# Kernel tuning notes

Measured on AMD Instinct MI355X. Metric: run time of the kernel, lower is better.

The kernel has to match this reference:

```python
import jax, jax.numpy as jnp
import numpy as np

N_NODES = 50000


def _gcn_layer(x, src, dst, norm_src, norm_dst, W, b, act):
    # DGL GraphConv with norm='both': D_out^{-1/2} A D_in^{-1/2} X W + b
    h = x * norm_src[:, None]                      # scale by src out-degree
    m = h[src]                                     # gather messages [E, d]
    agg = jax.ops.segment_sum(m, dst, num_segments=N_NODES)  # scatter-add
    agg = agg * norm_dst[:, None]
    out = agg @ W + b
    if act:
        out = jax.nn.relu(out)
    return out


def setup_inputs() -> dict:
    key = jax.random.key(0)
    ks = jax.random.split(key, 10)
    E = 800000
    in_size, hid, out_size = 128, 128, 64
    features = jax.random.normal(ks[0], (N_NODES, in_size), dtype=jnp.float32)
    src = jax.random.randint(ks[1], (E,), 0, N_NODES, dtype=jnp.int32)
    dst = jax.random.randint(ks[2], (E,), 0, N_NODES, dtype=jnp.int32)
    s = 0.05
    W1 = jax.random.normal(ks[3], (in_size, hid), dtype=jnp.float32) * s
    b1 = jnp.zeros((hid,), dtype=jnp.float32)
    W2 = jax.random.normal(ks[4], (hid, hid), dtype=jnp.float32) * s
    b2 = jnp.zeros((hid,), dtype=jnp.float32)
    W3 = jax.random.normal(ks[5], (hid, out_size), dtype=jnp.float32) * s
    b3 = jnp.zeros((out_size,), dtype=jnp.float32)
    return {"features": features, "W1": W1, "b1": b1, "W2": W2, "b2": b2,
            "W3": W3, "b3": b3, "src": src, "dst": dst}


def reference(features, W1, b1, W2, b2, W3, b3, src, dst):
    ones = jnp.ones(src.shape, dtype=features.dtype)
    out_deg = jax.ops.segment_sum(ones, src, num_segments=N_NODES)
    in_deg = jax.ops.segment_sum(ones, dst, num_segments=N_NODES)
    norm_src = jnp.maximum(out_deg, 1.0) ** -0.5   # clamp(min=1) as in DGL
    norm_dst = jnp.maximum(in_deg, 1.0) ** -0.5
    h = _gcn_layer(features, src, dst, norm_src, norm_dst, W1, b1, act=True)
    # dropout is identity in eval mode
    h = _gcn_layer(h, src, dst, norm_src, norm_dst, W2, b2, act=True)
    h = _gcn_layer(h, src, dst, norm_src, norm_dst, W3, b3, act=False)
    return h
```

## Files before the change

### kernel.cpp

```cpp
#include <hip/hip_runtime.h>
#include <math.h>

#define N_NODES 50000
#define K_DIM 128
#define CAP 64
#define CHUNK 25000
#define RH 25000
#define HWORDS 12500

typedef __attribute__((ext_vector_type(8))) short short8_t;
typedef __attribute__((ext_vector_type(4))) float f32x4_t;
typedef __attribute__((ext_vector_type(8))) _Float16 half8_t;

__device__ inline unsigned short f2bf(float x) {
    unsigned u = __float_as_uint(x);
    unsigned r = u + 0x7fffu + ((u >> 16) & 1u);
    return (unsigned short)(r >> 16);
}
__device__ inline float bf2f(unsigned short h) {
    return __uint_as_float(((unsigned)h) << 16);
}

__global__ void init_zero_kernel(_Float16* Yx, _Float16* Yy, _Float16* Yz) {
    int t = threadIdx.x;
    if (t < 128) {
        Yx[(size_t)N_NODES * 128 + t] = (_Float16)0.f;
        Yy[(size_t)N_NODES * 128 + t] = (_Float16)0.f;
    }
    if (t < 64) Yz[(size_t)N_NODES * 64 + t] = (_Float16)0.f;
}


__global__ __launch_bounds__(1024) void hist_kernel(const int* __restrict__ src,
                                                    const int* __restrict__ dst, int E,
                                                    unsigned* __restrict__ pin,
                                                    unsigned* __restrict__ pout) {
    __shared__ unsigned h[HWORDS];
    int b  = blockIdx.x >> 2;
    int io = (blockIdx.x >> 1) & 1;
    int r  = blockIdx.x & 1;
    int tid = threadIdx.x;
    for (int t = tid; t < HWORDS; t += 1024) h[t] = 0;
    __syncthreads();
    const int* keys = io ? src : dst;
    int start = b * CHUNK;
    int end = start + CHUNK; if (end > E) end = E;
    int vlo = r * RH;
    for (int i = start + tid; i < end; i += 1024) {
        int v = keys[i] - vlo;
        if ((unsigned)v < (unsigned)RH)
            atomicAdd(&h[v >> 1], 1u << ((v & 1) * 16));
    }
    __syncthreads();
    unsigned* out = io ? pout : pin;
    for (int t = tid; t < HWORDS; t += 1024)
        out[(size_t)b * (2 * HWORDS) + r * HWORDS + t] = h[t];
}

__global__ void offsets_norm_kernel(const unsigned* __restrict__ pin,
                                    const unsigned* __restrict__ pout,
                                    unsigned short* __restrict__ off16,
                                    int* __restrict__ indeg,
                                    float* __restrict__ nsrc, float* __restrict__ ndst,
                                    int n, int NB) {
    int v = blockIdx.x * blockDim.x + threadIdx.x;
    if (v >= n) return;
    int wi = v >> 1, sh = (v & 1) * 16;
    int od = 0;
    for (int b = 0; b < NB; ++b)
        od += (pout[(size_t)b * (2 * HWORDS) + wi] >> sh) & 0xffff;
    int run = 0;
    for (int b = 0; b < NB; ++b) {
        int c = (pin[(size_t)b * (2 * HWORDS) + wi] >> sh) & 0xffff;
        off16[(size_t)b * n + v] = (unsigned short)(run < CAP ? run : CAP);
        run += c;
    }
    indeg[v] = run < CAP ? run : CAP;
    int odc = od < 1 ? 1 : od;
    int idc = run < 1 ? 1 : run;
    nsrc[v] = 1.0f / sqrtf((float)odc);
    ndst[v] = 1.0f / sqrtf((float)idc);
}

__global__ __launch_bounds__(1024) void scatter_kernel(const int* __restrict__ src,
                                                       const int* __restrict__ dst, int E,
                                                       const unsigned short* __restrict__ off16,
                                                       int* __restrict__ csr, int n) {
    __shared__ unsigned cur[HWORDS];
    int b = blockIdx.x >> 1;
    int r = blockIdx.x & 1;
    int tid = threadIdx.x;
    int vlo = r * RH;
    const unsigned short* offb = off16 + (size_t)b * n + vlo;
    for (int t = tid; t < HWORDS; t += 1024)
        cur[t] = (unsigned)offb[2 * t] | ((unsigned)offb[2 * t + 1] << 16);
    __syncthreads();
    int start = b * CHUNK;
    int end = start + CHUNK; if (end > E) end = E;
    for (int i = start + tid; i < end; i += 1024) {
        int v = dst[i];
        int vr = v - vlo;
        if ((unsigned)vr < (unsigned)RH) {
            int sh = (vr & 1) * 16;
            unsigned old = atomicAdd(&cur[vr >> 1], 1u << sh);
            unsigned p = (old >> sh) & 0xffff;
            if (p < CAP) csr[((size_t)v << 6) + p] = src[i];
        }
    }
}

__global__ void split_w_all_kernel(const float* __restrict__ W1,
                                   const float* __restrict__ W2,
                                   const float* __restrict__ W3,
                                   unsigned short* __restrict__ W1h, unsigned short* __restrict__ W1l,
                                   unsigned short* __restrict__ W2h, unsigned short* __restrict__ W2l,
                                   unsigned short* __restrict__ W3h, unsigned short* __restrict__ W3l) {
    int gi = blockIdx.x * blockDim.x + threadIdx.x;
    const float* W; unsigned short *WBh, *WBl; int M, i;
    if (gi < 2048)      { W = W1; WBh = W1h; WBl = W1l; M = 128; i = gi; }
    else if (gi < 4096) { W = W2; WBh = W2h; WBl = W2l; M = 128; i = gi - 2048; }
    else if (gi < 5120) { W = W3; WBh = W3h; WBl = W3l; M = 64;  i = gi - 4096; }
    else return;
    int c    = i >> 8;
    int rem  = i & 255;
    int kc   = rem >> 6;
    int lane = rem & 63;
    int m = lane & 15, q = lane >> 4;
    int n = c * 16 + m;
    #pragma unroll
    for (int j = 0; j < 8; ++j) {
        int k = kc * 32 + q * 8 + j;
        float w = W[(size_t)k * M + n];
        unsigned short hi = f2bf(w);
        unsigned short lo = f2bf(w - bf2f(hi));
        WBh[(size_t)i * 8 + j] = hi;
        WBl[(size_t)i * 8 + j] = lo;
    }
}

template <int M>
__global__ __launch_bounds__(256) void gemm_mfma_kernel(
        const float* __restrict__ X,
        const unsigned short* __restrict__ WBh_,
        const unsigned short* __restrict__ WBl_,
        const float* __restrict__ nsrc, _Float16* __restrict__ Yh, int n) {
    constexpr int LSTR = 136;
    __shared__ short Xhi[64 * LSTR];
    __shared__ short Xlo[64 * LSTR];
    int tid = threadIdx.x;
    int lane = tid & 63, wave = tid >> 6;
    int rowBlock = blockIdx.x * 64;

    #pragma unroll
    for (int l = 0; l < 8; ++l) {
        int idx = (tid + l * 256) * 4;
        int r = idx >> 7;
        int c = idx & 127;
        float4 v = make_float4(0.f, 0.f, 0.f, 0.f);
        int gr = rowBlock + r;
        if (gr < n) v = *(const float4*)&X[(size_t)gr * K_DIM + c];
        unsigned short h0 = f2bf(v.x), h1 = f2bf(v.y), h2 = f2bf(v.z), h3 = f2bf(v.w);
        short4 hs = {(short)h0, (short)h1, (short)h2, (short)h3};
        short4 ls = {(short)f2bf(v.x - bf2f(h0)), (short)f2bf(v.y - bf2f(h1)),
                     (short)f2bf(v.z - bf2f(h2)), (short)f2bf(v.w - bf2f(h3))};
        *(short4*)&Xhi[r * LSTR + c] = hs;
        *(short4*)&Xlo[r * LSTR + c] = ls;
    }
    __syncthreads();

    int m = lane & 15, q = lane >> 4;
    short8_t ah[4], al[4];
    {
        int abase = (wave * 16 + m) * LSTR + q * 8;
        #pragma unroll
        for (int kc = 0; kc < 4; ++kc) {
            ah[kc] = *(const short8_t*)&Xhi[abase + kc * 32];
            al[kc] = *(const short8_t*)&Xlo[abase + kc * 32];
        }
    }
    float ns[4];
    int orow0 = rowBlock + wave * 16 + q * 4;
    #pragma unroll
    for (int r = 0; r < 4; ++r) ns[r] = (orow0 + r < n) ? nsrc[orow0 + r] : 0.f;

    const short8_t* WBh = (const short8_t*)WBh_;
    const short8_t* WBl = (const short8_t*)WBl_;
    constexpr int CT = M / 16;
    #pragma unroll
    for (int c = 0; c < CT; ++c) {
        short8_t bh[4], bl[4];
        #pragma unroll
        for (int kc = 0; kc < 4; ++kc) {
            bh[kc] = WBh[(c * 4 + kc) * 64 + lane];
            bl[kc] = WBl[(c * 4 + kc) * 64 + lane];
        }
        f32x4_t acc = {0.f, 0.f, 0.f, 0.f};
        #pragma unroll
        for (int kc = 0; kc < 4; ++kc) {
            acc = __builtin_amdgcn_mfma_f32_16x16x32_bf16(ah[kc], bh[kc], acc, 0, 0, 0);
            acc = __builtin_amdgcn_mfma_f32_16x16x32_bf16(ah[kc], bl[kc], acc, 0, 0, 0);
            acc = __builtin_amdgcn_mfma_f32_16x16x32_bf16(al[kc], bh[kc], acc, 0, 0, 0);
        }
        int col = c * 16 + m;
        #pragma unroll
        for (int r = 0; r < 4; ++r) {
            int row = orow0 + r;
            if (row < n) Yh[(size_t)row * M + col] = (_Float16)(acc[r] * ns[r]);
        }
    }
}

template <int MOUT>
__global__ __launch_bounds__(256) void agg_gemm_kernel(
        const _Float16* __restrict__ Yin,
        const int* __restrict__ indeg, const int* __restrict__ csr,
        const float* __restrict__ ndst, const float* __restrict__ bias,
        const unsigned short* __restrict__ WBh_,
        const unsigned short* __restrict__ WBl_,
        const float* __restrict__ nsrc, _Float16* __restrict__ Yout, int n) {
    constexpr int LSTR = 136;
    __shared__ short Xhi[64 * LSTR];
    __shared__ short Xlo[64 * LSTR];
    int tid = threadIdx.x;
    int lane = tid & 63, wave = tid >> 6;
    int rowBlock = blockIdx.x * 64;

    int sub = tid >> 4;
    int f8  = (tid & 15) * 8;
    #pragma unroll
    for (int p = 0; p < 4; ++p) {
        int r = p * 16 + sub;
        int v = rowBlock + r;
        float o[8] = {};
        if (v < n) {
            int deg = indeg[v];
            const int* __restrict__ row = &csr[(size_t)v * CAP];
            float acc[8] = {};
            for (int i = 0; i < deg; i += 4) {
                int4 ss = *(const int4*)&row[i];
                int s0 = ss.x;
                int s1 = (i + 1 < deg) ? ss.y : N_NODES;
                int s2 = (i + 2 < deg) ? ss.z : N_NODES;
                int s3 = (i + 3 < deg) ? ss.w : N_NODES;
                half8_t a = *(const half8_t*)&Yin[(size_t)s0 * 128 + f8];
                half8_t b = *(const half8_t*)&Yin[(size_t)s1 * 128 + f8];
                half8_t c = *(const half8_t*)&Yin[(size_t)s2 * 128 + f8];
                half8_t d = *(const half8_t*)&Yin[(size_t)s3 * 128 + f8];
                #pragma unroll
                for (int j = 0; j < 8; ++j)
                    acc[j] += ((float)a[j] + (float)b[j]) + ((float)c[j] + (float)d[j]);
            }
            float nd = ndst[v];
            #pragma unroll
            for (int j = 0; j < 8; ++j)
                o[j] = fmaxf(nd * acc[j] + bias[f8 + j], 0.f);
        }
        short hs[8], ls[8];
        #pragma unroll
        for (int j = 0; j < 8; ++j) {
            unsigned short h = f2bf(o[j]);
            hs[j] = (short)h;
            ls[j] = (short)f2bf(o[j] - bf2f(h));
        }
        *(short4*)&Xhi[r * LSTR + f8]     = *(short4*)&hs[0];
        *(short4*)&Xhi[r * LSTR + f8 + 4] = *(short4*)&hs[4];
        *(short4*)&Xlo[r * LSTR + f8]     = *(short4*)&ls[0];
        *(short4*)&Xlo[r * LSTR + f8 + 4] = *(short4*)&ls[4];
    }
    __syncthreads();

    int m = lane & 15, q = lane >> 4;
    short8_t ah[4], al[4];
    {
        int abase = (wave * 16 + m) * LSTR + q * 8;
        #pragma unroll
        for (int kc = 0; kc < 4; ++kc) {
            ah[kc] = *(const short8_t*)&Xhi[abase + kc * 32];
            al[kc] = *(const short8_t*)&Xlo[abase + kc * 32];
        }
    }
    float ns[4];
    int orow0 = rowBlock + wave * 16 + q * 4;
    #pragma unroll
    for (int r = 0; r < 4; ++r) ns[r] = (orow0 + r < n) ? nsrc[orow0 + r] : 0.f;

    const short8_t* WBh = (const short8_t*)WBh_;
    const short8_t* WBl = (const short8_t*)WBl_;
    constexpr int CT = MOUT / 16;
    #pragma unroll
    for (int c = 0; c < CT; ++c) {
        short8_t bh[4], bl[4];
        #pragma unroll
        for (int kc = 0; kc < 4; ++kc) {
            bh[kc] = WBh[(c * 4 + kc) * 64 + lane];
            bl[kc] = WBl[(c * 4 + kc) * 64 + lane];
        }
        f32x4_t acc = {0.f, 0.f, 0.f, 0.f};
        #pragma unroll
        for (int kc = 0; kc < 4; ++kc) {
            acc = __builtin_amdgcn_mfma_f32_16x16x32_bf16(ah[kc], bh[kc], acc, 0, 0, 0);
            acc = __builtin_amdgcn_mfma_f32_16x16x32_bf16(ah[kc], bl[kc], acc, 0, 0, 0);
            acc = __builtin_amdgcn_mfma_f32_16x16x32_bf16(al[kc], bh[kc], acc, 0, 0, 0);
        }
        int col = c * 16 + m;
        #pragma unroll
        for (int r = 0; r < 4; ++r) {
            int row = orow0 + r;
            if (row < n) Yout[(size_t)row * MOUT + col] = (_Float16)(acc[r] * ns[r]);
        }
    }
}

template <int M, bool RELU>
__global__ __launch_bounds__(256) void agg_kernel(const _Float16* __restrict__ Y,
                                                  const int* __restrict__ indeg,
                                                  const int* __restrict__ csr,
                                                  const float* __restrict__ ndst,
                                                  const float* __restrict__ bias,
                                                  float* __restrict__ Z, int n) {
    constexpr int LPN = M / 8;
    constexpr int NPB = 256 / LPN;
    int v = blockIdx.x * NPB + threadIdx.x / LPN;
    if (v >= n) return;
    int f8 = (threadIdx.x % LPN) * 8;
    int deg = indeg[v];
    const int* __restrict__ row = &csr[(size_t)v * CAP];
    float acc[8] = {};
    for (int i = 0; i < deg; i += 4) {
        int4 ss = *(const int4*)&row[i];
        int s0 = ss.x;
        int s1 = (i + 1 < deg) ? ss.y : N_NODES;
        int s2 = (i + 2 < deg) ? ss.z : N_NODES;
        int s3 = (i + 3 < deg) ? ss.w : N_NODES;
        half8_t a = *(const half8_t*)&Y[(size_t)s0 * M + f8];
        half8_t b = *(const half8_t*)&Y[(size_t)s1 * M + f8];
        half8_t c = *(const half8_t*)&Y[(size_t)s2 * M + f8];
        half8_t d = *(const half8_t*)&Y[(size_t)s3 * M + f8];
        #pragma unroll
        for (int j = 0; j < 8; ++j)
            acc[j] += ((float)a[j] + (float)b[j]) + ((float)c[j] + (float)d[j]);
    }
    float nd = ndst[v];
    float4 bb0 = *(const float4*)&bias[f8];
    float4 bb1 = *(const float4*)&bias[f8 + 4];
    float o[8];
    o[0] = nd * acc[0] + bb0.x; o[1] = nd * acc[1] + bb0.y;
    o[2] = nd * acc[2] + bb0.z; o[3] = nd * acc[3] + bb0.w;
    o[4] = nd * acc[4] + bb1.x; o[5] = nd * acc[5] + bb1.y;
    o[6] = nd * acc[6] + bb1.z; o[7] = nd * acc[7] + bb1.w;
    if (RELU) {
        #pragma unroll
        for (int j = 0; j < 8; ++j) o[j] = fmaxf(o[j], 0.f);
    }
    *(float4*)&Z[(size_t)v * M + f8]     = make_float4(o[0], o[1], o[2], o[3]);
    *(float4*)&Z[(size_t)v * M + f8 + 4] = make_float4(o[4], o[5], o[6], o[7]);
}


extern "C" void kernel_launch(void* const* d_in, const int* in_sizes, int n_in,
                              void* d_out, int out_size, void* d_ws, size_t ws_size,
                              hipStream_t stream) {
    const float* features = (const float*)d_in[0];
    const float* W1 = (const float*)d_in[1];
    const float* b1 = (const float*)d_in[2];
    const float* W2 = (const float*)d_in[3];
    const float* b2 = (const float*)d_in[4];
    const float* W3 = (const float*)d_in[5];
    const float* b3 = (const float*)d_in[6];
    const int* src = (const int*)d_in[7];
    const int* dst = (const int*)d_in[8];
    const int E = in_sizes[7];
    const int N = N_NODES;
    const int NB = (E + CHUNK - 1) / CHUNK;

    char* w = (char*)d_ws;
    auto alloc = [&](size_t bytes) {
        char* p = w;
        w += (bytes + 255) & ~(size_t)255;
        return p;
    };
    _Float16* Yx = (_Float16*)alloc((size_t)(N + 1) * 128 * 2);
    _Float16* Yy = (_Float16*)alloc((size_t)(N + 1) * 128 * 2);
    _Float16* Yz = (_Float16*)alloc((size_t)(N + 1) * 64 * 2);
    int*   csr    = (int*)alloc((size_t)N * CAP * 4);
    unsigned* pin  = (unsigned*)alloc((size_t)NB * 2 * HWORDS * 4);
    unsigned* pout = (unsigned*)alloc((size_t)NB * 2 * HWORDS * 4);
    unsigned short* off16 = (unsigned short*)alloc((size_t)NB * N * 2);
    int*   indeg  = (int*)alloc((size_t)N * 4);
    float* nsrc   = (float*)alloc((size_t)N * 4);
    float* ndst   = (float*)alloc((size_t)N * 4);
    unsigned short* W1h = (unsigned short*)alloc(128 * 128 * 2);
    unsigned short* W1l = (unsigned short*)alloc(128 * 128 * 2);
    unsigned short* W2h = (unsigned short*)alloc(128 * 128 * 2);
    unsigned short* W2l = (unsigned short*)alloc(128 * 128 * 2);
    unsigned short* W3h = (unsigned short*)alloc(64 * 128 * 2);
    unsigned short* W3l = (unsigned short*)alloc(64 * 128 * 2);

    init_zero_kernel<<<1, 128, 0, stream>>>(Yx, Yy, Yz);
    hist_kernel<<<NB * 4, 1024, 0, stream>>>(src, dst, E, pin, pout);
    offsets_norm_kernel<<<(N + 255) / 256, 256, 0, stream>>>(pin, pout, off16, indeg,
                                                             nsrc, ndst, N, NB);
    scatter_kernel<<<NB * 2, 1024, 0, stream>>>(src, dst, E, off16, csr, N);
    split_w_all_kernel<<<20, 256, 0, stream>>>(W1, W2, W3, W1h, W1l, W2h, W2l, W3h, W3l);

    int gblocks = (N + 63) / 64;
    gemm_mfma_kernel<128><<<gblocks, 256, 0, stream>>>(features, W1h, W1l, nsrc, Yx, N);
    agg_gemm_kernel<128><<<gblocks, 256, 0, stream>>>(Yx, indeg, csr, ndst, b1,
                                                      W2h, W2l, nsrc, Yy, N);
    agg_gemm_kernel<64><<<gblocks, 256, 0, stream>>>(Yy, indeg, csr, ndst, b2,
                                                     W3h, W3l, nsrc, Yz, N);
    agg_kernel<64, false><<<(N + 31) / 32, 256, 0, stream>>>(Yz, indeg, csr, ndst, b3,
                                                             (float*)d_out, N);
}
```

Measured before the change: 244.2 us.

## Split fused aggregate-GEMM into feature-slab aggregation and separate split-bf16 GEMM

Replaces the fused aggregate+GEMM kernels with a slab aggregation kernel and a standalone GEMM that reads pre-split bf16 hi/lo activations. The slab kernel gives each block a 32-feature column slice of the gathered table and a node range. The aim is for the per-slab working set of gathered rows to stay cache-resident, improving reuse in the random gathers. It also uses persistent grid-stride blocks and nontemporal loads and stores for the CSR and outputs. The cost is extra kernel launches and a round trip of the intermediate hi/lo arrays through global memory.

Measured after the change: 349.8 us. +43.2%, slower.

```diff
diff --git a/kernel.cpp b/kernel.cpp
--- a/kernel.cpp
+++ b/kernel.cpp
@@ -11,6 +11,7 @@
 typedef __attribute__((ext_vector_type(8))) short short8_t;
 typedef __attribute__((ext_vector_type(4))) float f32x4_t;
 typedef __attribute__((ext_vector_type(8))) _Float16 half8_t;
+typedef __attribute__((ext_vector_type(4))) int int32x4_t;
 
 __device__ inline unsigned short f2bf(float x) {
     unsigned u = __float_as_uint(x);
@@ -211,10 +212,9 @@
 }
 
 template <int MOUT>
-__global__ __launch_bounds__(256) void agg_gemm_kernel(
-        const _Float16* __restrict__ Yin,
-        const int* __restrict__ indeg, const int* __restrict__ csr,
-        const float* __restrict__ ndst, const float* __restrict__ bias,
+__global__ __launch_bounds__(256) void gemm_split_kernel(
+        const unsigned short* __restrict__ Zhi,
+        const unsigned short* __restrict__ Zlo,
         const unsigned short* __restrict__ WBh_,
         const unsigned short* __restrict__ WBl_,
         const float* __restrict__ nsrc, _Float16* __restrict__ Yout, int n) {
@@ -225,47 +225,19 @@
     int lane = tid & 63, wave = tid >> 6;
     int rowBlock = blockIdx.x * 64;
 
-    int sub = tid >> 4;
-    int f8  = (tid & 15) * 8;
-    #pragma unroll
-    for (int p = 0; p < 4; ++p) {
-        int r = p * 16 + sub;
-        int v = rowBlock + r;
-        float o[8] = {};
-        if (v < n) {
-            int deg = indeg[v];
-            const int* __restrict__ row = &csr[(size_t)v * CAP];
-            float acc[8] = {};
-            for (int i = 0; i < deg; i += 4) {
-                int4 ss = *(const int4*)&row[i];
-                int s0 = ss.x;
-                int s1 = (i + 1 < deg) ? ss.y : N_NODES;
-                int s2 = (i + 2 < deg) ? ss.z : N_NODES;
-                int s3 = (i + 3 < deg) ? ss.w : N_NODES;
-                half8_t a = *(const half8_t*)&Yin[(size_t)s0 * 128 + f8];
-                half8_t b = *(const half8_t*)&Yin[(size_t)s1 * 128 + f8];
-                half8_t c = *(const half8_t*)&Yin[(size_t)s2 * 128 + f8];
-                half8_t d = *(const half8_t*)&Yin[(size_t)s3 * 128 + f8];
-                #pragma unroll
-                for (int j = 0; j < 8; ++j)
-                    acc[j] += ((float)a[j] + (float)b[j]) + ((float)c[j] + (float)d[j]);
-            }
-            float nd = ndst[v];
-            #pragma unroll
-            for (int j = 0; j < 8; ++j)
-                o[j] = fmaxf(nd * acc[j] + bias[f8 + j], 0.f);
-        }
-        short hs[8], ls[8];
-        #pragma unroll
-        for (int j = 0; j < 8; ++j) {
-            unsigned short h = f2bf(o[j]);
-            hs[j] = (short)h;
-            ls[j] = (short)f2bf(o[j] - bf2f(h));
-        }
-        *(short4*)&Xhi[r * LSTR + f8]     = *(short4*)&hs[0];
-        *(short4*)&Xhi[r * LSTR + f8 + 4] = *(short4*)&hs[4];
-        *(short4*)&Xlo[r * LSTR + f8]     = *(short4*)&ls[0];
-        *(short4*)&Xlo[r * LSTR + f8 + 4] = *(short4*)&ls[4];
+    #pragma unroll
+    for (int l = 0; l < 4; ++l) {
+        int e = (tid + l * 256) * 8;
+        int r = e >> 7;
+        int c = e & 127;
+        int gr = rowBlock + r;
+        short8_t h = {0,0,0,0,0,0,0,0}, lo = {0,0,0,0,0,0,0,0};
+        if (gr < n) {
+            h  = *(const short8_t*)&Zhi[(size_t)gr * 128 + c];
+            lo = *(const short8_t*)&Zlo[(size_t)gr * 128 + c];
+        }
+        *(short8_t*)&Xhi[r * LSTR + c] = h;
+        *(short8_t*)&Xlo[r * LSTR + c] = lo;
     }
     __syncthreads();
 
@@ -311,49 +283,74 @@
     }
 }
 
-template <int M, bool RELU>
-__global__ __launch_bounds__(256) void agg_kernel(const _Float16* __restrict__ Y,
-                                                  const int* __restrict__ indeg,
-                                                  const int* __restrict__ csr,
-                                                  const float* __restrict__ ndst,
-                                                  const float* __restrict__ bias,
-                                                  float* __restrict__ Z, int n) {
-    constexpr int LPN = M / 8;
-    constexpr int NPB = 256 / LPN;
-    int v = blockIdx.x * NPB + threadIdx.x / LPN;
-    if (v >= n) return;
-    int f8 = (threadIdx.x % LPN) * 8;
-    int deg = indeg[v];
-    const int* __restrict__ row = &csr[(size_t)v * CAP];
-    float acc[8] = {};
-    for (int i = 0; i < deg; i += 4) {
-        int4 ss = *(const int4*)&row[i];
-        int s0 = ss.x;
-        int s1 = (i + 1 < deg) ? ss.y : N_NODES;
-        int s2 = (i + 2 < deg) ? ss.z : N_NODES;
-        int s3 = (i + 3 < deg) ? ss.w : N_NODES;
-        half8_t a = *(const half8_t*)&Y[(size_t)s0 * M + f8];
-        half8_t b = *(const half8_t*)&Y[(size_t)s1 * M + f8];
-        half8_t c = *(const half8_t*)&Y[(size_t)s2 * M + f8];
-        half8_t d = *(const half8_t*)&Y[(size_t)s3 * M + f8];
-        #pragma unroll
-        for (int j = 0; j < 8; ++j)
-            acc[j] += ((float)a[j] + (float)b[j]) + ((float)c[j] + (float)d[j]);
-    }
-    float nd = ndst[v];
+template <int MF, bool RELU, bool SPLIT_OUT>
+__global__ __launch_bounds__(256) void slab_agg_kernel(
+        const _Float16* __restrict__ Yin,
+        const int* __restrict__ indeg, const int* __restrict__ csr,
+        const float* __restrict__ ndst, const float* __restrict__ bias,
+        unsigned short* __restrict__ Zhi, unsigned short* __restrict__ Zlo,
+        float* __restrict__ Out, int n) {
+    constexpr int NSLAB = MF / 32;
+    constexpr int P = 8 / NSLAB;
+    constexpr int RANGE = N_NODES / P;
+    int x = blockIdx.x & 7;
+    int slab = x % NSLAB;
+    int part = x / NSLAB;
+    int jb = blockIdx.x >> 3;
+    int laneq = threadIdx.x & 3;
+    int nsub = threadIdx.x >> 2;
+    int f8 = slab * 32 + laneq * 8;
+    int base = part * RANGE;
     float4 bb0 = *(const float4*)&bias[f8];
     float4 bb1 = *(const float4*)&bias[f8 + 4];
-    float o[8];
-    o[0] = nd * acc[0] + bb0.x; o[1] = nd * acc[1] + bb0.y;
-    o[2] = nd * acc[2] + bb0.z; o[3] = nd * acc[3] + bb0.w;
-    o[4] = nd * acc[4] + bb1.x; o[5] = nd * acc[5] + bb1.y;
-    o[6] = nd * acc[6] + bb1.z; o[7] = nd * acc[7] + bb1.w;
-    if (RELU) {
-        #pragma unroll
-        for (int j = 0; j < 8; ++j) o[j] = fmaxf(o[j], 0.f);
-    }
-    *(float4*)&Z[(size_t)v * M + f8]     = make_float4(o[0], o[1], o[2], o[3]);
-    *(float4*)&Z[(size_t)v * M + f8 + 4] = make_float4(o[4], o[5], o[6], o[7]);
+
+    for (int v0 = jb * 64; v0 < RANGE; v0 += 64 * 64) {
+        int v = base + v0 + nsub;
+        if (v0 + nsub >= RANGE || v >= n) continue;
+        int deg = indeg[v];
+        const int* __restrict__ row = &csr[(size_t)v << 6];
+        float acc[8] = {};
+        for (int i = 0; i < deg; i += 4) {
+            int32x4_t ss = __builtin_nontemporal_load((const int32x4_t*)&row[i]);
+            int s0 = ss.x;
+            int s1 = (i + 1 < deg) ? ss.y : N_NODES;
+            int s2 = (i + 2 < deg) ? ss.z : N_NODES;
+            int s3 = (i + 3 < deg) ? ss.w : N_NODES;
+            half8_t a = *(const half8_t*)&Yin[(size_t)s0 * MF + f8];
+            half8_t b = *(const half8_t*)&Yin[(size_t)s1 * MF + f8];
+            half8_t c = *(const half8_t*)&Yin[(size_t)s2 * MF + f8];
+            half8_t d = *(const half8_t*)&Yin[(size_t)s3 * MF + f8];
+            #pragma unroll
+            for (int j = 0; j < 8; ++j)
+                acc[j] += ((float)a[j] + (float)b[j]) + ((float)c[j] + (float)d[j]);
+        }
+        float nd = ndst[v];
+        float o[8];
+        o[0] = nd * acc[0] + bb0.x; o[1] = nd * acc[1] + bb0.y;
+        o[2] = nd * acc[2] + bb0.z; o[3] = nd * acc[3] + bb0.w;
+        o[4] = nd * acc[4] + bb1.x; o[5] = nd * acc[5] + bb1.y;
+        o[6] = nd * acc[6] + bb1.z; o[7] = nd * acc[7] + bb1.w;
+        if (RELU) {
+            #pragma unroll
+            for (int j = 0; j < 8; ++j) o[j] = fmaxf(o[j], 0.f);
+        }
+        if (SPLIT_OUT) {
+            short8_t hs, ls;
+            #pragma unroll
+            for (int j = 0; j < 8; ++j) {
+                unsigned short h = f2bf(o[j]);
+                hs[j] = (short)h;
+                ls[j] = (short)f2bf(o[j] - bf2f(h));
+            }
+            __builtin_nontemporal_store(hs, (short8_t*)&Zhi[(size_t)v * MF + f8]);
+            __builtin_nontemporal_store(ls, (short8_t*)&Zlo[(size_t)v * MF + f8]);
+        } else {
+            f32x4_t o0 = {o[0], o[1], o[2], o[3]};
+            f32x4_t o1 = {o[4], o[5], o[6], o[7]};
+            __builtin_nontemporal_store(o0, (f32x4_t*)&Out[(size_t)v * MF + f8]);
+            __builtin_nontemporal_store(o1, (f32x4_t*)&Out[(size_t)v * MF + f8 + 4]);
+        }
+    }
 }
 
 
@@ -382,6 +379,8 @@
     _Float16* Yx = (_Float16*)alloc((size_t)(N + 1) * 128 * 2);
     _Float16* Yy = (_Float16*)alloc((size_t)(N + 1) * 128 * 2);
     _Float16* Yz = (_Float16*)alloc((size_t)(N + 1) * 64 * 2);
+    unsigned short* Zhi = (unsigned short*)alloc((size_t)N * 128 * 2);
+    unsigned short* Zlo = (unsigned short*)alloc((size_t)N * 128 * 2);
     int*   csr    = (int*)alloc((size_t)N * CAP * 4);
     unsigned* pin  = (unsigned*)alloc((size_t)NB * 2 * HWORDS * 4);
     unsigned* pout = (unsigned*)alloc((size_t)NB * 2 * HWORDS * 4);
@@ -404,11 +403,14 @@
     split_w_all_kernel<<<20, 256, 0, stream>>>(W1, W2, W3, W1h, W1l, W2h, W2l, W3h, W3l);
 
     int gblocks = (N + 63) / 64;
+    const int SLAB_GRID = 512;
     gemm_mfma_kernel<128><<<gblocks, 256, 0, stream>>>(features, W1h, W1l, nsrc, Yx, N);
-    agg_gemm_kernel<128><<<gblocks, 256, 0, stream>>>(Yx, indeg, csr, ndst, b1,
-                                                      W2h, W2l, nsrc, Yy, N);
-    agg_gemm_kernel<64><<<gblocks, 256, 0, stream>>>(Yy, indeg, csr, ndst, b2,
-                                                     W3h, W3l, nsrc, Yz, N);
-    agg_kernel<64, false><<<(N + 31) / 32, 256, 0, stream>>>(Yz, indeg, csr, ndst, b3,
-                                                             (float*)d_out, N);
-}
+    slab_agg_kernel<128, true, true><<<SLAB_GRID, 256, 0, stream>>>(
+        Yx, indeg, csr, ndst, b1, Zhi, Zlo, nullptr, N);
+    gemm_split_kernel<128><<<gblocks, 256, 0, stream>>>(Zhi, Zlo, W2h, W2l, nsrc, Yy, N);
+    slab_agg_kernel<128, true, true><<<SLAB_GRID, 256, 0, stream>>>(
+        Yy, indeg, csr, ndst, b2, Zhi, Zlo, nullptr, N);
+    gemm_split_kernel<64><<<gblocks, 256, 0, stream>>>(Zhi, Zlo, W3h, W3l, nsrc, Yz, N);
+    slab_agg_kernel<64, false, false><<<SLAB_GRID, 256, 0, stream>>>(
+        Yz, indeg, csr, ndst, b3, nullptr, nullptr, (float*)d_out, N);
+}
```
